# Optimization experiments

Measured on AMD Instinct MI355X. Metric: run time of the kernel, lower is better.

The kernel has to match this reference:

```python
import jax, jax.numpy as jnp
import numpy as np

N = 100000
E = 3200000
F_IN = 128
H = 64


def _glorot(key, fan_in, fan_out):
    lim = jnp.sqrt(6.0 / (fan_in + fan_out))
    return jax.random.uniform(key, (fan_in, fan_out), minval=-lim, maxval=lim, dtype=jnp.float32)


def setup_inputs() -> dict:
    key = jax.random.key(0)
    ks = jax.random.split(key, 16)
    x = jax.random.normal(ks[0], (N, F_IN), dtype=jnp.float32)
    edge_index = jax.random.randint(ks[1], (2, E), 0, N, dtype=jnp.int32)
    batch = jnp.zeros((N,), dtype=jnp.int32)
    dims = [(F_IN, H), (H, H // 2), (H // 2, H // 4), (H // 4, H // 2), (H // 2, H), (H, F_IN)]
    params = {}
    for i, (fi, fo) in enumerate(dims):
        params[f"W{i+1}"] = _glorot(ks[2 + i], fi, fo)
        params[f"b{i+1}"] = jnp.zeros((fo,), dtype=jnp.float32)
    params["Wf"] = _glorot(ks[10], F_IN, F_IN)
    params["bf"] = jnp.zeros((F_IN,), dtype=jnp.float32)
    return {"x": x, "edge_index": edge_index, "batch": batch, **params}


def _gcn_norm(edge_index, num_nodes):
    # PyG GCNConv: add self-loops, sym-normalize with deg^{-1/2}
    loop = jnp.arange(num_nodes, dtype=edge_index.dtype)
    row = jnp.concatenate([edge_index[0], loop])  # source j
    col = jnp.concatenate([edge_index[1], loop])  # target i
    deg = jax.ops.segment_sum(jnp.ones_like(col, dtype=jnp.float32), col, num_segments=num_nodes)
    dinv = jnp.where(deg > 0, jax.lax.rsqrt(deg), 0.0)
    norm = dinv[row] * dinv[col]
    return row, col, norm


def _gcn_conv(h, W, b, row, col, norm, num_nodes):
    h = h @ W  # linear first (no bias in lin), then normalized scatter-add
    msg = h[row] * norm[:, None]
    agg = jax.ops.segment_sum(msg, col, num_segments=num_nodes)
    return agg + b


def reference(x, edge_index, batch, W1, b1, W2, b2, W3, b3, W4, b4, W5, b5, W6, b6, Wf, bf):
    n = x.shape[0]
    row, col, norm = _gcn_norm(edge_index, n)
    h = jax.nn.relu(_gcn_conv(x, W1, b1, row, col, norm, n))
    h = jax.nn.relu(_gcn_conv(h, W2, b2, row, col, norm, n))
    h = jax.nn.relu(_gcn_conv(h, W3, b3, row, col, norm, n))
    h = jax.nn.relu(_gcn_conv(h, W4, b4, row, col, norm, n))
    h = jax.nn.relu(_gcn_conv(h, W5, b5, row, col, norm, n))
    h = jax.nn.relu(_gcn_conv(h, W6, b6, row, col, norm, n))
    return h @ Wf + bf
```

## Files before the change

### kernel.cpp

```cpp
#include <hip/hip_runtime.h>
#include <hip/hip_fp16.h>

#define BLK 256
#define NBSHIFT 9
#define MAXNB 200
#define GPART 512

__device__ __forceinline__ float4 ld4(const float* p) { return *(const float4*)p; }

__global__ __launch_bounds__(BLK) void p1_hist_k(const int* __restrict__ cols, int* __restrict__ hist,
                                                 int E, int nb) {
    __shared__ int h[MAXNB];
    const int tid = threadIdx.x, g = blockIdx.x;
    for (int b = tid; b < nb; b += BLK) h[b] = 0;
    __syncthreads();
    const int chunk = (E + GPART - 1) / GPART;
    const int start = g * chunk, end = min(E, start + chunk);
    for (int e = start + tid; e < end; e += BLK) atomicAdd(&h[cols[e] >> NBSHIFT], 1);
    __syncthreads();
    for (int b = tid; b < nb; b += BLK) hist[b * GPART + g] = h[b];
}
__global__ __launch_bounds__(256) void p2a_k(const int* __restrict__ hist, int* __restrict__ bstart,
                                             int nb, int E) {
    __shared__ int s[256];
    const int t = threadIdx.x;
    int tot = 0;
    if (t < nb) {
        const int* hp = &hist[t * GPART];
        for (int g = 0; g < GPART; g++) tot += hp[g];
    }
    s[t] = tot;
    __syncthreads();
    for (int o = 1; o < 256; o <<= 1) {
        int v = s[t] + ((t >= o) ? s[t - o] : 0);
        __syncthreads();
        s[t] = v;
        __syncthreads();
    }
    if (t < nb) bstart[t] = s[t] - tot;
    if (t == 0) bstart[nb] = E;
}
__global__ __launch_bounds__(256) void p2b_k(int* __restrict__ hist, const int* __restrict__ bstart) {
    __shared__ int s[GPART];
    const int b = blockIdx.x, t = threadIdx.x;
    const int v0 = hist[b * GPART + t], v1 = hist[b * GPART + 256 + t];
    s[t] = v0; s[256 + t] = v1;
    __syncthreads();
    for (int o = 1; o < GPART; o <<= 1) {
        const int a0 = s[t] + ((t >= o) ? s[t - o] : 0);
        const int a1 = s[256 + t] + ((256 + t >= o) ? s[256 + t - o] : 0);
        __syncthreads();
        s[t] = a0; s[256 + t] = a1;
        __syncthreads();
    }
    const int base = bstart[b];
    hist[b * GPART + t] = base + s[t] - v0;
    hist[b * GPART + 256 + t] = base + s[256 + t] - v1;
}
__global__ __launch_bounds__(BLK) void p3_part_k(const int* __restrict__ rows, const int* __restrict__ cols,
                                                 const int* __restrict__ hist, int2* __restrict__ pairs,
                                                 int E, int nb) {
    __shared__ int tail[MAXNB];
    const int tid = threadIdx.x, g = blockIdx.x;
    for (int b = tid; b < nb; b += BLK) tail[b] = hist[b * GPART + g];
    __syncthreads();
    const int chunk = (E + GPART - 1) / GPART;
    const int start = g * chunk, end = min(E, start + chunk);
    for (int e = start + tid; e < end; e += BLK) {
        const int r = rows[e], c = cols[e];
        const int pos = atomicAdd(&tail[c >> NBSHIFT], 1);
        pairs[pos] = make_int2(r, c);
    }
}
__global__ __launch_bounds__(BLK) void p4_fill_k(const int2* __restrict__ pairs, const int* __restrict__ bstart,
                                                 int* __restrict__ P, float* __restrict__ dinv,
                                                 int* __restrict__ srow, int n) {
    __shared__ int dh[1 << NBSHIFT];
    __shared__ int tl[1 << NBSHIFT];
    const int b = blockIdx.x, t = threadIdx.x;
    const int base = b << NBSHIFT;
    const int nnod = min(1 << NBSHIFT, n - base);
    const int lo = bstart[b], hi = bstart[b + 1];
    dh[t] = 0; dh[256 + t] = 0;
    __syncthreads();
    for (int e = lo + t; e < hi; e += BLK) atomicAdd(&dh[pairs[e].y - base], 1);
    __syncthreads();
    const int v0 = dh[t], v1 = dh[256 + t];
    tl[t] = v0; tl[256 + t] = v1;
    __syncthreads();
    for (int o = 1; o < (1 << NBSHIFT); o <<= 1) {
        const int a0 = tl[t] + ((t >= o) ? tl[t - o] : 0);
        const int a1 = tl[256 + t] + ((256 + t >= o) ? tl[256 + t - o] : 0);
        __syncthreads();
        tl[t] = a0; tl[256 + t] = a1;
        __syncthreads();
    }
    const int s0 = lo + tl[t] - v0;
    const int s1 = lo + tl[256 + t] - v1;
    __syncthreads();
    tl[t] = s0; tl[256 + t] = s1;
    if (t < nnod)       { P[base + t] = s0;       dinv[base + t] = rsqrtf((float)v0 + 1.0f); }
    if (256 + t < nnod) { P[base + 256 + t] = s1; dinv[base + 256 + t] = rsqrtf((float)v1 + 1.0f); }
    __syncthreads();
    for (int e = lo + t; e < hi; e += BLK) {
        const int2 pr = pairs[e];
        const int pos = atomicAdd(&tl[pr.y - base], 1);
        srow[pos] = pr.x;
    }
}

__device__ __forceinline__ void addh(float2 A[4], const __half* p) {
    const float4 raw = ld4((const float*)p);
    const __half2* h = (const __half2*)&raw;
    const float2 f0 = __half22float2(h[0]);
    const float2 f1 = __half22float2(h[1]);
    const float2 f2 = __half22float2(h[2]);
    const float2 f3 = __half22float2(h[3]);
    A[0].x += f0.x; A[0].y += f0.y;
    A[1].x += f1.x; A[1].y += f1.y;
    A[2].x += f2.x; A[2].y += f2.y;
    A[3].x += f3.x; A[3].y += f3.y;
}

template<int WD, bool PRE, bool OUTH>
__global__ __launch_bounds__(BLK) void gatherh_k(const __half* __restrict__ Tp, const int* __restrict__ P,
                                                 const int* __restrict__ srow, const float* __restrict__ dinv,
                                                 const float* __restrict__ bin, void* __restrict__ outv,
                                                 int n, int E) {
    constexpr int LPN = WD / 8;
    const long gid = (long)blockIdx.x * BLK + threadIdx.x;
    const int i = (int)(gid / LPN);
    if (i >= n) return;
    const int q = (int)(gid % LPN) * 8;
    const int start = P[i];
    const int end = (i + 1 < n) ? P[i + 1] : E;
    const float d = dinv[i];
    const __half* __restrict__ Tq = Tp + q;
    float2 A0[4], A1[4], A2[4], A3[4];
    {
        const float4 raw = ld4((const float*)(Tq + (long)i * WD));
        const __half2* h = (const __half2*)&raw;
        A0[0] = __half22float2(h[0]); A0[1] = __half22float2(h[1]);
        A0[2] = __half22float2(h[2]); A0[3] = __half22float2(h[3]);
    }
#pragma unroll
    for (int k = 0; k < 4; k++) {
        A1[k] = make_float2(0.f, 0.f); A2[k] = make_float2(0.f, 0.f); A3[k] = make_float2(0.f, 0.f);
    }
    int e = start;
    const int ea = min(end, (start + 3) & ~3);
    for (; e < ea; e++) addh(A0, Tq + (long)srow[e] * WD);
    for (; e + 8 <= end; e += 8) {
        const int4 j0 = *(const int4*)&srow[e];
        const int4 j1 = *(const int4*)&srow[e + 4];
        addh(A0, Tq + (long)j0.x * WD); addh(A1, Tq + (long)j0.y * WD);
        addh(A2, Tq + (long)j0.z * WD); addh(A3, Tq + (long)j0.w * WD);
        addh(A0, Tq + (long)j1.x * WD); addh(A1, Tq + (long)j1.y * WD);
        addh(A2, Tq + (long)j1.z * WD); addh(A3, Tq + (long)j1.w * WD);
    }
    if (e + 4 <= end) {
        const int4 j0 = *(const int4*)&srow[e];
        addh(A0, Tq + (long)j0.x * WD); addh(A1, Tq + (long)j0.y * WD);
        addh(A2, Tq + (long)j0.z * WD); addh(A3, Tq + (long)j0.w * WD);
        e += 4;
    }
    for (; e < end; e++) addh(A0, Tq + (long)srow[e] * WD);
#pragma unroll
    for (int k = 0; k < 4; k++) {
        A0[k].x += A1[k].x + A2[k].x + A3[k].x;
        A0[k].y += A1[k].y + A2[k].y + A3[k].y;
    }
    float v[8];
    v[0] = d * A0[0].x; v[1] = d * A0[0].y; v[2] = d * A0[1].x; v[3] = d * A0[1].y;
    v[4] = d * A0[2].x; v[5] = d * A0[2].y; v[6] = d * A0[3].x; v[7] = d * A0[3].y;
    if (PRE) {
        const float4 b0 = ld4(&bin[q]);
        const float4 b1 = ld4(&bin[q + 4]);
        v[0] = fmaxf(v[0] + b0.x, 0.f) * d; v[1] = fmaxf(v[1] + b0.y, 0.f) * d;
        v[2] = fmaxf(v[2] + b0.z, 0.f) * d; v[3] = fmaxf(v[3] + b0.w, 0.f) * d;
        v[4] = fmaxf(v[4] + b1.x, 0.f) * d; v[5] = fmaxf(v[5] + b1.y, 0.f) * d;
        v[6] = fmaxf(v[6] + b1.z, 0.f) * d; v[7] = fmaxf(v[7] + b1.w, 0.f) * d;
    }
    if (OUTH) {
        const __half2 h0 = __floats2half2_rn(v[0], v[1]);
        const __half2 h1 = __floats2half2_rn(v[2], v[3]);
        const __half2 h2 = __floats2half2_rn(v[4], v[5]);
        const __half2 h3 = __floats2half2_rn(v[6], v[7]);
        uint4 u;
        u.x = *(const unsigned int*)&h0; u.y = *(const unsigned int*)&h1;
        u.z = *(const unsigned int*)&h2; u.w = *(const unsigned int*)&h3;
        *(uint4*)((__half*)outv + (long)i * WD + q) = u;
    } else {
        float* out = (float*)outv;
        float4 v0, v1;
        v0.x = v[0]; v0.y = v[1]; v0.z = v[2]; v0.w = v[3];
        v1.x = v[4]; v1.y = v[5]; v1.z = v[6]; v1.w = v[7];
        *(float4*)&out[(long)i * WD + q] = v0;
        *(float4*)&out[(long)i * WD + q + 4] = v1;
    }
}

template<int FI, int FO, bool INB, bool OUTB, bool OUTRELU, bool OSC, bool OUTH>
__global__ __launch_bounds__(BLK) void gemm_k(const float* __restrict__ H, const float* __restrict__ Wm,
                                              const float* __restrict__ bin, const float* __restrict__ bout,
                                              const float* __restrict__ dinv, float* __restrict__ out, int n) {
    constexpr int COLT = FO / 4;
    constexpr int RTH  = BLK / COLT;
    constexpr int RPT  = (FO >= 64) ? 8 : 4;
    constexpr int ROWS = RTH * RPT;
    constexpr int KC   = (FI > 64) ? 64 : FI;
    constexpr int NKB  = FI / KC;

    __shared__ float Wl[KC * FO];
    __shared__ float Hl[ROWS * (KC + 1)];

    const int tid    = threadIdx.x;
    const int colIdx = tid % COLT;
    const int rowIdx = tid / COLT;
    const long rowBase = (long)blockIdx.x * ROWS;

    float4 acc[RPT];
#pragma unroll
    for (int i = 0; i < RPT; i++) acc[i] = make_float4(0.f, 0.f, 0.f, 0.f);

    for (int kb = 0; kb < NKB; kb++) {
        if (kb) __syncthreads();
        for (int f = tid * 4; f < KC * FO; f += BLK * 4) {
            const int kr = f / FO, c = f % FO;
            *(float4*)&Wl[kr * FO + c] = ld4(&Wm[(kb * KC + kr) * FO + c]);
        }
        for (int f = tid * 4; f < ROWS * KC; f += BLK * 4) {
            const int rr = f / KC, kk = f % KC;
            const long r = rowBase + rr;
            float4 v = make_float4(0.f, 0.f, 0.f, 0.f);
            if (r < n) v = ld4(&H[r * FI + kb * KC + kk]);
            if (INB) {
                float4 b4 = ld4(&bin[kb * KC + kk]);
                v.x = fmaxf(v.x + b4.x, 0.f); v.y = fmaxf(v.y + b4.y, 0.f);
                v.z = fmaxf(v.z + b4.z, 0.f); v.w = fmaxf(v.w + b4.w, 0.f);
            }
            float* dst = &Hl[rr * (KC + 1) + kk];
            dst[0] = v.x; dst[1] = v.y; dst[2] = v.z; dst[3] = v.w;
        }
        __syncthreads();
#pragma unroll 8
        for (int k = 0; k < KC; k++) {
            const float4 w4 = *(const float4*)&Wl[k * FO + 4 * colIdx];
#pragma unroll
            for (int i = 0; i < RPT; i++) {
                const float hv = Hl[(rowIdx * RPT + i) * (KC + 1) + k];
                acc[i].x = fmaf(hv, w4.x, acc[i].x);
                acc[i].y = fmaf(hv, w4.y, acc[i].y);
                acc[i].z = fmaf(hv, w4.z, acc[i].z);
                acc[i].w = fmaf(hv, w4.w, acc[i].w);
            }
        }
    }

    float4 bo = make_float4(0.f, 0.f, 0.f, 0.f);
    if (OUTB) bo = ld4(&bout[4 * colIdx]);
#pragma unroll
    for (int i = 0; i < RPT; i++) {
        const long r = rowBase + rowIdx * RPT + i;
        if (r < n) {
            float4 v = acc[i];
            if (OUTB) { v.x += bo.x; v.y += bo.y; v.z += bo.z; v.w += bo.w; }
            if (OUTRELU) {
                v.x = fmaxf(v.x, 0.f); v.y = fmaxf(v.y, 0.f);
                v.z = fmaxf(v.z, 0.f); v.w = fmaxf(v.w, 0.f);
            }
            if (OSC) {
                const float d = dinv[r];
                v.x *= d; v.y *= d; v.z *= d; v.w *= d;
            }
            if (OUTH) {
                const __half2 h01 = __floats2half2_rn(v.x, v.y);
                const __half2 h23 = __floats2half2_rn(v.z, v.w);
                uint2 u;
                u.x = *(const unsigned int*)&h01;
                u.y = *(const unsigned int*)&h23;
                *(uint2*)((__half*)out + r * FO + 4 * colIdx) = u;
            } else {
                *(float4*)&out[r * FO + 4 * colIdx] = v;
            }
        }
    }
}

extern "C" void kernel_launch(void* const* d_in, const int* in_sizes, int n_in,
                              void* d_out, int out_size, void* d_ws, size_t ws_size,
                              hipStream_t stream)
{
    const float* x  = (const float*)d_in[0];
    const int*   ei = (const int*)d_in[1];
    const float* W1 = (const float*)d_in[3];  const float* b1 = (const float*)d_in[4];
    const float* W2 = (const float*)d_in[5];  const float* b2 = (const float*)d_in[6];
    const float* W3 = (const float*)d_in[7];  const float* b3 = (const float*)d_in[8];
    const float* W4 = (const float*)d_in[9];  const float* b4 = (const float*)d_in[10];
    const float* W5 = (const float*)d_in[11]; const float* b5 = (const float*)d_in[12];
    const float* W6 = (const float*)d_in[13]; const float* b6 = (const float*)d_in[14];
    const float* Wf = (const float*)d_in[15]; const float* bf = (const float*)d_in[16];

    const int n = in_sizes[0] / 128;
    const int E = in_sizes[1] / 2;
    const int* rows = ei;
    const int* cols = ei + E;

    int*   P    = (int*)d_ws;
    int*   srow = P + n;
    float* dinv = (float*)(srow + E);
    float* bufA = dinv + n;
    float* bufB = bufA + (size_t)n * 128;
    int2*  pairs = (int2*)bufA;
    int*   hist  = (int*)bufB;
    int*   bstart= hist + MAXNB * GPART;

    auto cdiv = [](long a, long b) { return (unsigned)((a + b - 1) / b); };
    const int nb = (n + (1 << NBSHIFT) - 1) >> NBSHIFT;

    p1_hist_k<<<GPART, BLK, 0, stream>>>(cols, hist, E, nb);
    p2a_k<<<1, 256, 0, stream>>>(hist, bstart, nb, E);
    p2b_k<<<nb, 256, 0, stream>>>(hist, bstart);
    p3_part_k<<<GPART, BLK, 0, stream>>>(rows, cols, hist, pairs, E, nb);
    p4_fill_k<<<nb, BLK, 0, stream>>>(pairs, bstart, P, dinv, srow, n);

    gemm_k<128, 64, false, false, false, true, true><<<cdiv(n, 128), BLK, 0, stream>>>(x, W1, nullptr, nullptr, dinv, bufA, n);
    gatherh_k<64, false, false><<<cdiv((long)n * 8, BLK), BLK, 0, stream>>>((const __half*)bufA, P, srow, dinv, nullptr, bufB, n, E);

    gemm_k<64, 32, true, false, false, true, true><<<cdiv(n, 128), BLK, 0, stream>>>(bufB, W2, b1, nullptr, dinv, bufA, n);
    gatherh_k<32, false, false><<<cdiv((long)n * 4, BLK), BLK, 0, stream>>>((const __half*)bufA, P, srow, dinv, nullptr, bufB, n, E);

    gemm_k<32, 16, true, false, false, true, true><<<cdiv(n, 256), BLK, 0, stream>>>(bufB, W3, b2, nullptr, dinv, bufA, n);
    gatherh_k<16, true, true><<<cdiv((long)n * 2, BLK), BLK, 0, stream>>>((const __half*)bufA, P, srow, dinv, b3, bufB, n, E);

    gatherh_k<16, false, false><<<cdiv((long)n * 2, BLK), BLK, 0, stream>>>((const __half*)bufB, P, srow, dinv, nullptr, bufA, n, E);
    gemm_k<16, 32, false, true, true, true, true><<<cdiv(n, 128), BLK, 0, stream>>>(bufA, W4, nullptr, b4, dinv, bufB, n);

    gatherh_k<32, false, false><<<cdiv((long)n * 4, BLK), BLK, 0, stream>>>((const __half*)bufB, P, srow, dinv, nullptr, bufA, n, E);
    gemm_k<32, 64, false, true, true, true, true><<<cdiv(n, 128), BLK, 0, stream>>>(bufA, W5, nullptr, b5, dinv, bufB, n);

    gatherh_k<64, false, false><<<cdiv((long)n * 8, BLK), BLK, 0, stream>>>((const __half*)bufB, P, srow, dinv, nullptr, bufA, n, E);
    gemm_k<64, 128, false, true, true, false, false><<<cdiv(n, 64), BLK, 0, stream>>>(bufA, W6, nullptr, b6, nullptr, bufB, n);

    gemm_k<128, 128, false, true, false, false, false><<<cdiv(n, 64), BLK, 0, stream>>>(bufB, Wf, nullptr, bf, nullptr, (float*)d_out, n);
}
```

Measured before the change: 684.9 us.

## Use MFMA fp16 GEMM kernel for wide layers with half intermediates

Adds an MFMA-based GEMM kernel that stages fp16 A and B tiles in LDS and uses 16x16x32 f16 matrix instructions. It replaces the scalar GEMMs for layer 1, layer 6 and the final projection. The last gather now writes half output, and the layer-6 result is stored as half, which halves the memory traffic of those intermediates. This trades fp32 precision on the input conversion and intermediates for fewer bytes moved and tensor-core throughput, and the output stores are scalar and strided.

```diff
diff --git a/kernel.cpp b/kernel.cpp
--- a/kernel.cpp
+++ b/kernel.cpp
@@ -5,6 +5,10 @@
 #define NBSHIFT 9
 #define MAXNB 200
 #define GPART 512
+
+typedef _Float16 half4v __attribute__((ext_vector_type(4)));
+typedef _Float16 half8v __attribute__((ext_vector_type(8)));
+typedef float    f32x4v __attribute__((ext_vector_type(4)));
 
 __device__ __forceinline__ float4 ld4(const float* p) { return *(const float4*)p; }
 
@@ -287,6 +291,105 @@
     }
 }
 
+template<int K, int FO, bool AH, bool OUTB, bool OUTRELU, bool OSC, bool OUTH>
+__global__ __launch_bounds__(BLK) void mgemm_k(const void* __restrict__ Hv, const float* __restrict__ Wm,
+                                               const float* __restrict__ bout, const float* __restrict__ dinv,
+                                               void* __restrict__ outv, int n) {
+    constexpr int BM = 128;
+    constexpr int KP = K + 8;
+    constexpr int NT = FO / 16;
+    __shared__ _Float16 Al[BM * KP];
+    __shared__ _Float16 Bl[FO * KP];
+
+    const int tid = threadIdx.x;
+    const long rowBase = (long)blockIdx.x * BM;
+
+    for (int f = tid * 4; f < K * FO; f += BLK * 4) {
+        const int nn = f / K, k0 = f % K;
+        const int blk = k0 & ~31, g = (k0 >> 2) & 3, h = (k0 >> 4) & 1;
+        half4v w4;
+#pragma unroll
+        for (int c = 0; c < 4; c++) w4[c] = (_Float16)Wm[(k0 + c) * FO + nn];
+        *(half4v*)&Bl[nn * KP + blk + 8 * g + 4 * h] = w4;
+    }
+    if (AH) {
+        const __half* Hp = (const __half*)Hv;
+        for (int f = tid * 8; f < BM * K; f += BLK * 8) {
+            const int rr = f / K, k0 = f % K;
+            const long r = rowBase + rr;
+            uint4 u = make_uint4(0u, 0u, 0u, 0u);
+            if (r < n) u = *(const uint4*)&Hp[r * K + k0];
+            const int blk = k0 & ~31, g0 = (k0 >> 2) & 3, h = (k0 >> 4) & 1;
+            *(uint2*)&Al[rr * KP + blk + 8 * g0 + 4 * h] = make_uint2(u.x, u.y);
+            *(uint2*)&Al[rr * KP + blk + 8 * (g0 + 1) + 4 * h] = make_uint2(u.z, u.w);
+        }
+    } else {
+        const float* Hp = (const float*)Hv;
+        for (int f = tid * 4; f < BM * K; f += BLK * 4) {
+            const int rr = f / K, k0 = f % K;
+            const long r = rowBase + rr;
+            float4 v = make_float4(0.f, 0.f, 0.f, 0.f);
+            if (r < n) v = ld4(&Hp[r * K + k0]);
+            const int blk = k0 & ~31, g = (k0 >> 2) & 3, h = (k0 >> 4) & 1;
+            half4v a4;
+            a4[0] = (_Float16)v.x; a4[1] = (_Float16)v.y; a4[2] = (_Float16)v.z; a4[3] = (_Float16)v.w;
+            *(half4v*)&Al[rr * KP + blk + 8 * g + 4 * h] = a4;
+        }
+    }
+    __syncthreads();
+
+    const int wv = tid >> 6;
+    const int lane = tid & 63;
+    const int lr = lane & 15;
+    const int lg = lane >> 4;
+    const int wrow = wv * 32;
+
+    const f32x4v vzero = {0.f, 0.f, 0.f, 0.f};
+    f32x4v acc[2][NT];
+#pragma unroll
+    for (int a = 0; a < 2; a++)
+#pragma unroll
+        for (int t = 0; t < NT; t++) acc[a][t] = vzero;
+
+#pragma unroll
+    for (int ks = 0; ks < K / 32; ks++) {
+        const int ko = ks * 32 + 8 * lg;
+        const half8v a0 = *(const half8v*)&Al[(wrow + lr) * KP + ko];
+        const half8v a1 = *(const half8v*)&Al[(wrow + 16 + lr) * KP + ko];
+#pragma unroll
+        for (int nt = 0; nt < NT; nt++) {
+            const half8v b = *(const half8v*)&Bl[(nt * 16 + lr) * KP + ko];
+            acc[0][nt] = __builtin_amdgcn_mfma_f32_16x16x32_f16(a0, b, acc[0][nt], 0, 0, 0);
+            acc[1][nt] = __builtin_amdgcn_mfma_f32_16x16x32_f16(a1, b, acc[1][nt], 0, 0, 0);
+        }
+    }
+
+    float bo[NT];
+    if (OUTB) {
+#pragma unroll
+        for (int nt = 0; nt < NT; nt++) bo[nt] = bout[nt * 16 + lr];
+    }
+#pragma unroll
+    for (int rt = 0; rt < 2; rt++) {
+#pragma unroll
+        for (int r = 0; r < 4; r++) {
+            const long row = rowBase + wrow + rt * 16 + lg * 4 + r;
+            if (row < n) {
+                const float d = OSC ? dinv[row] : 1.0f;
+#pragma unroll
+                for (int nt = 0; nt < NT; nt++) {
+                    float v = acc[rt][nt][r];
+                    if (OUTB) v += bo[nt];
+                    if (OUTRELU) v = fmaxf(v, 0.f);
+                    if (OSC) v *= d;
+                    if (OUTH) ((__half*)outv)[row * FO + nt * 16 + lr] = __float2half_rn(v);
+                    else      ((float*)outv)[row * FO + nt * 16 + lr] = v;
+                }
+            }
+        }
+    }
+}
+
 extern "C" void kernel_launch(void* const* d_in, const int* in_sizes, int n_in,
                               void* d_out, int out_size, void* d_ws, size_t ws_size,
                               hipStream_t stream)
@@ -324,7 +427,7 @@
     p3_part_k<<<GPART, BLK, 0, stream>>>(rows, cols, hist, pairs, E, nb);
     p4_fill_k<<<nb, BLK, 0, stream>>>(pairs, bstart, P, dinv, srow, n);
 
-    gemm_k<128, 64, false, false, false, true, true><<<cdiv(n, 128), BLK, 0, stream>>>(x, W1, nullptr, nullptr, dinv, bufA, n);
+    mgemm_k<128, 64, false, false, false, true, true><<<cdiv(n, 128), BLK, 0, stream>>>(x, W1, nullptr, dinv, bufA, n);
     gatherh_k<64, false, false><<<cdiv((long)n * 8, BLK), BLK, 0, stream>>>((const __half*)bufA, P, srow, dinv, nullptr, bufB, n, E);
 
     gemm_k<64, 32, true, false, false, true, true><<<cdiv(n, 128), BLK, 0, stream>>>(bufB, W2, b1, nullptr, dinv, bufA, n);
@@ -339,8 +442,8 @@
     gatherh_k<32, false, false><<<cdiv((long)n * 4, BLK), BLK, 0, stream>>>((const __half*)bufB, P, srow, dinv, nullptr, bufA, n, E);
     gemm_k<32, 64, false, true, true, true, true><<<cdiv(n, 128), BLK, 0, stream>>>(bufA, W5, nullptr, b5, dinv, bufB, n);
 
-    gatherh_k<64, false, false><<<cdiv((long)n * 8, BLK), BLK, 0, stream>>>((const __half*)bufB, P, srow, dinv, nullptr, bufA, n, E);
-    gemm_k<64, 128, false, true, true, false, false><<<cdiv(n, 64), BLK, 0, stream>>>(bufA, W6, nullptr, b6, nullptr, bufB, n);
-
-    gemm_k<128, 128, false, true, false, false, false><<<cdiv(n, 64), BLK, 0, stream>>>(bufB, Wf, nullptr, bf, nullptr, (float*)d_out, n);
-}
+    gatherh_k<64, false, true><<<cdiv((long)n * 8, BLK), BLK, 0, stream>>>((const __half*)bufB, P, srow, dinv, nullptr, bufA, n, E);
+    mgemm_k<64, 128, true, true, true, false, true><<<cdiv(n, 128), BLK, 0, stream>>>(bufA, W6, b6, nullptr, bufB, n);
+
+    mgemm_k<128, 128, true, true, false, false, false><<<cdiv(n, 128), BLK, 0, stream>>>(bufB, Wf, bf, nullptr, d_out, n);
+}
```

After: 664.7 us. 1.03x faster.
